# Optimization experiments

Hardware: AMD Instinct MI355X
Metric: run time of the kernel (lower is better)

## Reference

```python
import jax, jax.numpy as jnp
import numpy as np

N_MET, N_RXN, N_GENE = 2534, 4881, 6607
E, P, D = 262144, 131072, 256
LN_EPS = 1e-5


def _segment_mean(x, idx, n):
    s = jax.ops.segment_sum(x, idx, num_segments=n)
    c = jax.ops.segment_sum(jnp.ones((idx.shape[0],), x.dtype), idx, num_segments=n)
    return s / jnp.maximum(c, 1.0)[:, None]


def _hyperconv(x, eattr, node, edge, stoich, W, We, att, b):
    # PyG-style HypergraphConv with stoichiometry as incidence weight + attention.
    xp = x @ W                      # [N_MET, D]
    ep = eattr @ We                 # [N_RXN, D]
    xi = xp[node]                   # [E, D] gather
    ej = ep[edge]                   # [E, D] gather
    logits = jax.nn.leaky_relu(jnp.concatenate([xi, ej], axis=-1) @ att, 0.2)  # [E]
    m = jax.ops.segment_max(logits, edge, num_segments=N_RXN)
    ex = jnp.exp(logits - m[edge])
    ssum = jax.ops.segment_sum(ex, edge, num_segments=N_RXN)
    alpha = ex / (ssum[edge] + 1e-16)           # softmax per hyperedge
    w = stoich * alpha                           # [E]
    ones = jnp.ones_like(stoich)
    Bc = jax.ops.segment_sum(ones, edge, num_segments=N_RXN)   # nodes per edge
    me = jax.ops.segment_sum(w[:, None] * xi, edge, num_segments=N_RXN)
    me = me / jnp.maximum(Bc, 1.0)[:, None]      # node -> hyperedge
    Dc = jax.ops.segment_sum(ones, node, num_segments=N_MET)   # edges per node
    out = jax.ops.segment_sum(w[:, None] * me[edge], node, num_segments=N_MET)
    out = out / jnp.maximum(Dc, 1.0)[:, None]    # hyperedge -> node
    return out + b


def _layernorm(z, g, b):
    mu = jnp.mean(z, axis=-1, keepdims=True)
    var = jnp.mean(jnp.square(z - mu), axis=-1, keepdims=True)
    return (z - mu) / jnp.sqrt(var + LN_EPS) * g + b


def _renorm(emb):
    # nn.Embedding(max_norm=1.0): clamp row norms to <= 1
    n = jnp.linalg.norm(emb, axis=-1, keepdims=True)
    return emb * jnp.minimum(1.0, 1.0 / (n + 1e-12))


def setup_inputs() -> dict:
    key = jax.random.key(0)
    ks = jax.random.split(key, 16)
    s = 1.0 / np.sqrt(D)
    return {
        "he_node": jax.random.randint(ks[0], (E,), 0, N_MET),
        "he_edge": jax.random.randint(ks[1], (E,), 0, N_RXN),
        "stoich": jax.random.normal(ks[2], (E,), dtype=jnp.float32),
        "gene_x": jax.random.normal(ks[3], (N_GENE, D), dtype=jnp.float32),
        "rtg_rxn": jax.random.randint(ks[4], (P,), 0, N_RXN),
        "rtg_gene": jax.random.randint(ks[5], (P,), 0, N_GENE),
        "emb_table": jax.random.normal(ks[6], (N_MET, D), dtype=jnp.float32) * 0.02,
        "W0": jax.random.normal(ks[7], (D, D), dtype=jnp.float32) * s,
        "We0": jax.random.normal(ks[8], (D, D), dtype=jnp.float32) * s,
        "att0": jax.random.normal(ks[9], (2 * D,), dtype=jnp.float32) * s,
        "b0": jnp.zeros((D,), jnp.float32),
        "W1": jax.random.normal(ks[10], (D, D), dtype=jnp.float32) * s,
        "We1": jax.random.normal(ks[11], (D, D), dtype=jnp.float32) * s,
        "att1": jax.random.normal(ks[12], (2 * D,), dtype=jnp.float32) * s,
        "b1": jnp.zeros((D,), jnp.float32),
        "ln_g": jnp.ones((D,), jnp.float32),
        "ln_b": jnp.zeros((D,), jnp.float32),
    }


def reference(he_node, he_edge, stoich, gene_x, rtg_rxn, rtg_gene, emb_table,
              W0, We0, att0, b0, W1, We1, att1, b1, ln_g, ln_b):
    met = _renorm(emb_table)                                    # [N_MET, D]
    # gene -> reaction scatter-mean (flattened reaction_to_genes dict)
    rxn_emb = _segment_mean(gene_x[rtg_gene], rtg_rxn, N_RXN)   # [N_RXN, D]
    # layer 0 (no skip on first layer)
    cur = jnp.tanh(_hyperconv(met, rxn_emb, he_node, he_edge, stoich, W0, We0, att0, b0))
    # layer 1 with skip + layernorm
    nxt = jnp.tanh(_hyperconv(cur, rxn_emb, he_node, he_edge, stoich, W1, We1, att1, b1))
    cur = _layernorm(nxt + cur, ln_g, ln_b)
    # metabolite -> reaction scatter-mean over incidences
    rxn_final = _segment_mean(cur[he_node], he_edge, N_RXN)     # [N_RXN, D]
    # reaction -> gene scatter-mean
    gene_emb = _segment_mean(rxn_final[rtg_rxn], rtg_gene, N_GENE)  # [N_GENE, D]
    return gene_emb
```

## Files before the change

kernel.cpp:

```cpp
#include <hip/hip_runtime.h>
#include <math.h>

#define DD 256
static constexpr int N_MET  = 2534;
static constexpr int N_RXN  = 4881;
static constexpr int N_GENE = 6607;
static constexpr int NE     = 262144;
static constexpr int NP     = 131072;

static constexpr int NCHUNK = 256;
static constexpr int NBE    = 77;
static constexpr int NBN    = 80;
static constexpr int CHS    = 80;
static constexpr int GEMM_BLOCKS = (N_MET + 15) / 16;

__device__ __forceinline__ float waveSum(float v) {
  #pragma unroll
  for (int o = 32; o > 0; o >>= 1) v += __shfl_xor(v, o, 64);
  return v;
}
__device__ __forceinline__ float waveMax(float v) {
  #pragma unroll
  for (int o = 32; o > 0; o >>= 1) v = fmaxf(v, __shfl_xor(v, o, 64));
  return v;
}
__device__ __forceinline__ int   bcasti(int v, int l)   { return __builtin_amdgcn_readlane(v, l); }
__device__ __forceinline__ float bcastf(float v, int l) {
  return __int_as_float(__builtin_amdgcn_readlane(__float_as_int(v), l));
}

__global__ __launch_bounds__(1024) void KH_k(
    const int* __restrict__ he_node, const int* __restrict__ he_edge,
    const int* __restrict__ rtg_rxn, const int* __restrict__ rtg_gene,
    int* cntE, int* cntN, int* cntR, int* cntG,
    int* __restrict__ chE, int* __restrict__ chN,
    const float* __restrict__ We0, const float* __restrict__ att0,
    const float* __restrict__ We1, const float* __restrict__ att1,
    float* __restrict__ ve0, float* __restrict__ ve1) {
  int blk = blockIdx.x, tid = threadIdx.x;
  if (blk < 32) {
    int wid = blk * 16 + (tid >> 6);
    int lane = tid & 63;
    const float* We = (wid < 256) ? We0 : We1;
    const float* at = (wid < 256) ? att0 : att1;
    int r = wid & 255;
    float4 a = ((const float4*)(We + (size_t)r * DD))[lane];
    float4 v = ((const float4*)(at + DD))[lane];
    float s = waveSum(a.x * v.x + a.y * v.y + a.z * v.z + a.w * v.w);
    if (lane == 0) ((wid < 256) ? ve0 : ve1)[r] = s;
    return;
  }
  int c = blk - 32;
  __shared__ int hE[NBE], hN[NBN];
  if (tid < NBE) hE[tid] = 0;
  if (tid >= 128 && tid < 128 + NBN) hN[tid - 128] = 0;
  __syncthreads();
  int i = c * 1024 + tid;
  int n = he_node[i], e = he_edge[i];
  atomicAdd(&cntE[e], 1); atomicAdd(&cntN[n], 1);
  atomicAdd(&hE[e >> 6], 1); atomicAdd(&hN[n >> 5], 1);
  if (i < NP) { atomicAdd(&cntR[rtg_rxn[i]], 1); atomicAdd(&cntG[rtg_gene[i]], 1); }
  __syncthreads();
  if (tid < NBE) chE[c * CHS + tid] = hE[tid];
  if (tid >= 128 && tid < 128 + NBN) chN[c * CHS + (tid - 128)] = hN[tid - 128];
}

__global__ __launch_bounds__(1024) void KScan_k(
    const int* c0, int n0, int* o0, int* u0,
    const int* c1, int n1, int* o1, int* u1,
    const int* c2, int n2, int* o2, int* u2,
    const int* c3, int n3, int* o3, int* u3,
    int* __restrict__ chE, int* __restrict__ chN,
    const float* __restrict__ gene_x,
    const float* __restrict__ ve0, const float* __restrict__ ve1,
    float* __restrict__ gdot0, float* __restrict__ gdot1) {
  int blk = blockIdx.x, tid = threadIdx.x;
  if (blk < 4) {
    const int* cnt; int n; int* offs; int* cur;
    if      (blk == 0) { cnt = c0; n = n0; offs = o0; cur = u0; }
    else if (blk == 1) { cnt = c1; n = n1; offs = o1; cur = u1; }
    else if (blk == 2) { cnt = c2; n = n2; offs = o2; cur = u2; }
    else               { cnt = c3; n = n3; offs = o3; cur = u3; }
    __shared__ int part[1024];
    int base = tid * 8;
    int v[8]; int s = 0;
    #pragma unroll
    for (int j = 0; j < 8; ++j) { int x = (base + j < n) ? cnt[base + j] : 0; v[j] = x; s += x; }
    part[tid] = s;
    __syncthreads();
    for (int o = 1; o < 1024; o <<= 1) {
      int t = (tid >= o) ? part[tid - o] : 0;
      __syncthreads();
      part[tid] += t;
      __syncthreads();
    }
    int ex = part[tid] - s;
    #pragma unroll
    for (int j = 0; j < 8; ++j) {
      if (base + j < n) { offs[base + j] = ex; cur[base + j] = ex; ex += v[j]; }
    }
    if (tid == 1023) offs[n] = part[1023];
    return;
  }
  if (blk < 14) {
    int colw = (blk - 4) * 16 + (tid >> 6);
    int lane = tid & 63;
    if (colw >= 160) return;
    int side = colw >= 80;
    int b = colw - side * 80;
    int* ch = side ? chN : chE;
    int v[4]; int s = 0;
    int cbase = lane * 4;
    #pragma unroll
    for (int k = 0; k < 4; ++k) { v[k] = ch[(cbase + k) * CHS + b]; s += v[k]; }
    int inc = s;
    #pragma unroll
    for (int o = 1; o < 64; o <<= 1) { int t = __shfl_up(inc, o, 64); if (lane >= o) inc += t; }
    int ex = inc - s;
    #pragma unroll
    for (int k = 0; k < 4; ++k) { int t = v[k]; ch[(cbase + k) * CHS + b] = ex; ex += t; }
    return;
  }
  int wid = (blk - 14) * 16 + (tid >> 6);
  int lane = tid & 63;
  if (wid >= N_GENE) return;
  float4 a  = ((const float4*)gene_x)[(size_t)wid * 64 + lane];
  float4 v0 = ((const float4*)ve0)[lane];
  float4 v1 = ((const float4*)ve1)[lane];
  float s0 = waveSum(a.x * v0.x + a.y * v0.y + a.z * v0.z + a.w * v0.w);
  float s1 = waveSum(a.x * v1.x + a.y * v1.y + a.z * v1.z + a.w * v1.w);
  if (lane == 0) { gdot0[wid] = s0; gdot1[wid] = s1; }
}

__global__ __launch_bounds__(1024) void KP1_k(
    const int* __restrict__ he_node, const int* __restrict__ he_edge,
    const float* __restrict__ stoich,
    const int* __restrict__ offsE, const int* __restrict__ offsN,
    const int* __restrict__ chE, const int* __restrict__ chN,
    int4* __restrict__ scrE, int4* __restrict__ scrN,
    const int* __restrict__ rtg_rxn, const int* __restrict__ rtg_gene,
    int* curR, int* __restrict__ geneR,
    int* curG, int* __restrict__ rxnG) {
  int blk = blockIdx.x, tid = threadIdx.x;
  if (blk < NCHUNK) {
    __shared__ int cursE[NBE], cursN[NBN];
    int c = blk;
    if (tid < NBE) cursE[tid] = offsE[64 * tid] + chE[c * CHS + tid];
    if (tid >= 128 && tid < 128 + NBN) {
      int t = tid - 128;
      cursN[t] = offsN[32 * t] + chN[c * CHS + t];
    }
    __syncthreads();
    int i = c * 1024 + tid;
    int n = he_node[i], e = he_edge[i];
    int st = __float_as_int(stoich[i]);
    int dE = atomicAdd(&cursE[e >> 6], 1);
    scrE[dE] = make_int4(e, n, st, 0);
    int dN = atomicAdd(&cursN[n >> 5], 1);
    scrN[dN] = make_int4(n, e, st, 0);
  } else {
    int i = (blk - NCHUNK) * 1024 + tid;
    int r = rtg_rxn[i], g = rtg_gene[i];
    int pa = atomicAdd(&curR[r], 1); geneR[pa] = g;
    int pb = atomicAdd(&curG[g], 1); rxnG[pb] = r;
  }
}

template <bool RENORM>
__device__ __forceinline__ void gemm_body(const float* __restrict__ X,
                                          const float* __restrict__ W,
                                          const float* __restrict__ att,
                                          float* __restrict__ Y,
                                          float* __restrict__ sn, int M, int r0) {
  __shared__ float Xs[256][20];
  __shared__ float red[4][16];
  __shared__ float scl[16];
  int tid = threadIdx.x;
  int w = tid >> 6, lane = tid & 63;
  float xv[16];
  #pragma unroll
  for (int i = 0; i < 16; ++i) {
    int r = r0 + i;
    xv[i] = (r < M) ? X[(size_t)r * DD + tid] : 0.f;
  }
  if (RENORM) {
    #pragma unroll
    for (int i = 0; i < 16; ++i) {
      float v = waveSum(xv[i] * xv[i]);
      if (lane == 0) red[w][i] = v;
    }
    __syncthreads();
    if (tid < 16) {
      float t = red[0][tid] + red[1][tid] + red[2][tid] + red[3][tid];
      scl[tid] = fminf(1.f, 1.f / (sqrtf(t) + 1e-12f));
    }
    __syncthreads();
    #pragma unroll
    for (int i = 0; i < 16; ++i) xv[i] *= scl[i];
  }
  #pragma unroll
  for (int i = 0; i < 16; ++i) Xs[tid][i] = xv[i];
  __syncthreads();
  float acc[16];
  #pragma unroll
  for (int i = 0; i < 16; ++i) acc[i] = 0.f;
  const float* wp = W + tid;
  #pragma unroll 8
  for (int k = 0; k < 256; ++k) {
    float wv = wp[(size_t)k * DD];
    const float4* xr = reinterpret_cast<const float4*>(&Xs[k][0]);
    float4 a0 = xr[0], a1 = xr[1], a2 = xr[2], a3 = xr[3];
    acc[0]  += a0.x * wv; acc[1]  += a0.y * wv; acc[2]  += a0.z * wv; acc[3]  += a0.w * wv;
    acc[4]  += a1.x * wv; acc[5]  += a1.y * wv; acc[6]  += a1.z * wv; acc[7]  += a1.w * wv;
    acc[8]  += a2.x * wv; acc[9]  += a2.y * wv; acc[10] += a2.z * wv; acc[11] += a2.w * wv;
    acc[12] += a3.x * wv; acc[13] += a3.y * wv; acc[14] += a3.z * wv; acc[15] += a3.w * wv;
  }
  #pragma unroll
  for (int i = 0; i < 16; ++i) {
    int r = r0 + i;
    if (r < M) Y[(size_t)r * DD + tid] = acc[i];
  }
  float av = att[tid];
  __syncthreads();
  #pragma unroll
  for (int i = 0; i < 16; ++i) {
    float v = waveSum(acc[i] * av);
    if (lane == 0) red[w][i] = v;
  }
  __syncthreads();
  if (tid < 16) {
    int r = r0 + tid;
    if (r < M) sn[r] = red[0][tid] + red[1][tid] + red[2][tid] + red[3][tid];
  }
}

__global__ __launch_bounds__(256) void KP2_k(
    const int* __restrict__ offsE, const int* __restrict__ offsN,
    const int4* __restrict__ scrE, const int4* __restrict__ scrN,
    int2* __restrict__ payE, int2* __restrict__ payN,
    const float* __restrict__ emb, const float* __restrict__ W0,
    const float* __restrict__ att0, float* __restrict__ xp, float* __restrict__ sn) {
  int blk = blockIdx.x, tid = threadIdx.x;
  if (blk < NBE) {
    __shared__ int curs[64];
    int b = blk;
    int elo = 64 * b;
    int ecnt = min(64, N_RXN - elo);
    if (tid < ecnt) curs[tid] = offsE[elo + tid];
    __syncthreads();
    int lo = offsE[elo], hi = offsE[elo + ecnt];
    for (int j = lo + tid; j < hi; j += 256) {
      int4 r = scrE[j];
      int slot = atomicAdd(&curs[r.x - elo], 1);
      payE[slot] = make_int2(r.y, r.z);
    }
  } else if (blk < NBE + NBN) {
    __shared__ int curs[32];
    int b = blk - NBE;
    int nlo = 32 * b;
    int ncnt = min(32, N_MET - nlo);
    if (tid < ncnt) curs[tid] = offsN[nlo + tid];
    __syncthreads();
    int lo = offsN[nlo], hi = offsN[nlo + ncnt];
    for (int j = lo + tid; j < hi; j += 256) {
      int4 r = scrN[j];
      int slot = atomicAdd(&curs[r.x - nlo], 1);
      payN[slot] = make_int2(r.y, r.z);
    }
  } else {
    gemm_body<true>(emb, W0, att0, xp, sn, N_MET, (blk - NBE - NBN) * 16);
  }
}

__global__ __launch_bounds__(256) void gemm1_k(const float* __restrict__ X,
                                               const float* __restrict__ W,
                                               const float* __restrict__ att,
                                               float* __restrict__ Y,
                                               float* __restrict__ sn, int M) {
  gemm_body<false>(X, W, att, Y, sn, M, blockIdx.x * 16);
}

__device__ __forceinline__ void gatherAcc(float4& acc, const float4* __restrict__ src4,
                                          const int (&rv)[4], const float (&wv)[4],
                                          int nc, int lane) {
  #pragma unroll
  for (int c = 0; c < 4; ++c) {
    int lim = nc - c * 64; if (lim > 64) lim = 64;
    for (int t = 0; t < lim; t += 16) {
      float4 a[16]; float w[16];
      #pragma unroll
      for (int q = 0; q < 16; ++q) {
        int   n = bcasti(rv[c], t + q);
        w[q]    = bcastf(wv[c], t + q);
        a[q]    = src4[(size_t)n * 64 + lane];
      }
      #pragma unroll
      for (int q = 0; q < 16; ++q) {
        acc.x += w[q] * a[q].x; acc.y += w[q] * a[q].y;
        acc.z += w[q] * a[q].z; acc.w += w[q] * a[q].w;
      }
    }
  }
}

template <int STRIDE>
__global__ __launch_bounds__(256) void seg_mean_k(const int* __restrict__ offs,
                                                  const int* __restrict__ pay,
                                                  const float* __restrict__ src,
                                                  float* __restrict__ dst, int nseg) {
  int wid = (blockIdx.x * 256 + threadIdx.x) >> 6;
  int lane = threadIdx.x & 63;
  if (wid >= nseg) return;
  int beg = offs[wid], end = offs[wid + 1];
  int cnt = end - beg;
  int nc = cnt < 256 ? cnt : 256;
  int rv[4]; float wv[4];
  #pragma unroll
  for (int c = 0; c < 4; ++c) {
    int j = c * 64 + lane;
    if (j < nc) { rv[c] = pay[(size_t)(beg + j) * STRIDE]; wv[c] = 1.f; }
    else        { rv[c] = 0;                               wv[c] = 0.f; }
  }
  float4 acc = make_float4(0.f, 0.f, 0.f, 0.f);
  gatherAcc(acc, (const float4*)src, rv, wv, nc, lane);
  for (int j = 256; j < cnt; ++j) {
    int n = pay[(size_t)(beg + j) * STRIDE];
    float4 a = ((const float4*)src)[(size_t)n * 64 + lane];
    acc.x += a.x; acc.y += a.y; acc.z += a.z; acc.w += a.w;
  }
  float inv = 1.f / (float)(cnt > 1 ? cnt : 1);
  float4 o; o.x = acc.x * inv; o.y = acc.y * inv; o.z = acc.z * inv; o.w = acc.w * inv;
  ((float4*)dst)[(size_t)wid * 64 + lane] = o;
}

__global__ __launch_bounds__(256) void me_k(const int* __restrict__ offs,
                                            const int2* __restrict__ payE,
                                            const float* __restrict__ sn,
                                            const int* __restrict__ offsR,
                                            const int* __restrict__ geneR,
                                            const float* __restrict__ gdot,
                                            const float* __restrict__ xp,
                                            float* __restrict__ me,
                                            float4* __restrict__ rstat) {
  int wid = (blockIdx.x * 256 + threadIdx.x) >> 6;
  int lane = threadIdx.x & 63;
  if (wid >= N_RXN) return;
  int rb = offsR[wid], re = offsR[wid + 1];
  float sacc = 0.f;
  for (int j = rb + lane; j < re; j += 64) sacc += gdot[geneR[j]];
  int rc = re - rb;
  float ser = waveSum(sacc) / (float)(rc > 1 ? rc : 1);

  int beg = offs[wid], end = offs[wid + 1];
  int cnt = end - beg;
  int nc = cnt < 256 ? cnt : 256;
  int nv[4]; float wv[4]; float stv[4];
  float lmax = -1e30f;
  #pragma unroll
  for (int c = 0; c < 4; ++c) {
    int j = c * 64 + lane;
    if (j < nc) {
      int2 p = payE[beg + j];
      float l = sn[p.x] + ser;
      l = (l >= 0.f) ? l : 0.2f * l;
      nv[c] = p.x; wv[c] = l; stv[c] = __int_as_float(p.y);
      lmax = fmaxf(lmax, l);
    } else { nv[c] = 0; wv[c] = -1e30f; stv[c] = 0.f; }
  }
  for (int j = 256 + lane; j < cnt; j += 64) {
    int2 p = payE[beg + j];
    float l = sn[p.x] + ser;
    l = (l >= 0.f) ? l : 0.2f * l;
    lmax = fmaxf(lmax, l);
  }
  float m = waveMax(lmax);
  float s = 0.f;
  #pragma unroll
  for (int c = 0; c < 4; ++c) {
    if (c * 64 + lane < nc) { float e = expf(wv[c] - m); wv[c] = e; s += e; }
    else wv[c] = 0.f;
  }
  for (int j = 256 + lane; j < cnt; j += 64) {
    int2 p = payE[beg + j];
    float l = sn[p.x] + ser;
    l = (l >= 0.f) ? l : 0.2f * l;
    s += expf(l - m);
  }
  s = waveSum(s);
  float invS = 1.f / (s + 1e-16f);
  #pragma unroll
  for (int c = 0; c < 4; ++c) {
    if (c * 64 + lane < nc) wv[c] = stv[c] * wv[c] * invS;
  }
  if (lane == 0) rstat[wid] = make_float4(ser, m, invS, 0.f);
  float4 acc = make_float4(0.f, 0.f, 0.f, 0.f);
  gatherAcc(acc, (const float4*)xp, nv, wv, nc, lane);
  for (int j = 256; j < cnt; ++j) {
    int2 p = payE[beg + j];
    float l = sn[p.x] + ser;
    l = (l >= 0.f) ? l : 0.2f * l;
    float w = __int_as_float(p.y) * expf(l - m) * invS;
    float4 a = ((const float4*)xp)[(size_t)p.x * 64 + lane];
    acc.x += w * a.x; acc.y += w * a.y; acc.z += w * a.z; acc.w += w * a.w;
  }
  float invB = 1.f / (float)(cnt > 1 ? cnt : 1);
  float4 o; o.x = acc.x * invB; o.y = acc.y * invB; o.z = acc.z * invB; o.w = acc.w * invB;
  ((float4*)me)[(size_t)wid * 64 + lane] = o;
}

template <bool LN>
__global__ __launch_bounds__(256) void out_k(const int* __restrict__ offs,
                                             const int2* __restrict__ payN,
                                             const float* __restrict__ sn,
                                             const float4* __restrict__ rstat,
                                             const float* __restrict__ me,
                                             const float* __restrict__ bias,
                                             const float* __restrict__ ln_g,
                                             const float* __restrict__ ln_b,
                                             float* __restrict__ cur) {
  int wid = (blockIdx.x * 256 + threadIdx.x) >> 6;
  int lane = threadIdx.x & 63;
  if (wid >= N_MET) return;
  int beg = offs[wid], end = offs[wid + 1];
  int cnt = end - beg;
  int nc = cnt < 256 ? cnt : 256;
  float sn_n = sn[wid];
  int rv[4]; float wv[4];
  #pragma unroll
  for (int c = 0; c < 4; ++c) {
    int j = c * 64 + lane;
    if (j < nc) {
      int2 p = payN[beg + j];
      float4 st = rstat[p.x];
      float l = sn_n + st.x;
      l = (l >= 0.f) ? l : 0.2f * l;
      rv[c] = p.x;
      wv[c] = __int_as_float(p.y) * expf(l - st.y) * st.z;
    } else { rv[c] = 0; wv[c] = 0.f; }
  }
  float4 acc = make_float4(0.f, 0.f, 0.f, 0.f);
  gatherAcc(acc, (const float4*)me, rv, wv, nc, lane);
  for (int j = 256; j < cnt; ++j) {
    int2 p = payN[beg + j];
    float4 st = rstat[p.x];
    float l = sn_n + st.x;
    l = (l >= 0.f) ? l : 0.2f * l;
    float w = __int_as_float(p.y) * expf(l - st.y) * st.z;
    float4 a = ((const float4*)me)[(size_t)p.x * 64 + lane];
    acc.x += w * a.x; acc.y += w * a.y; acc.z += w * a.z; acc.w += w * a.w;
  }
  float invD = 1.f / (float)(cnt > 1 ? cnt : 1);
  float4 b4 = ((const float4*)bias)[lane];
  float4 o;
  o.x = tanhf(acc.x * invD + b4.x);
  o.y = tanhf(acc.y * invD + b4.y);
  o.z = tanhf(acc.z * invD + b4.z);
  o.w = tanhf(acc.w * invD + b4.w);
  float4* cur4 = (float4*)cur;
  if (!LN) {
    cur4[(size_t)wid * 64 + lane] = o;
    return;
  }
  float4 p = cur4[(size_t)wid * 64 + lane];
  float4 z; z.x = o.x + p.x; z.y = o.y + p.y; z.z = o.z + p.z; z.w = o.w + p.w;
  float mu = waveSum(z.x + z.y + z.z + z.w) * (1.f / 256.f);
  float4 zc; zc.x = z.x - mu; zc.y = z.y - mu; zc.z = z.z - mu; zc.w = z.w - mu;
  float var = waveSum(zc.x * zc.x + zc.y * zc.y + zc.z * zc.z + zc.w * zc.w) * (1.f / 256.f);
  float rs = 1.f / sqrtf(var + 1e-5f);
  float4 g4 = ((const float4*)ln_g)[lane];
  float4 be4 = ((const float4*)ln_b)[lane];
  float4 r;
  r.x = zc.x * rs * g4.x + be4.x;
  r.y = zc.y * rs * g4.y + be4.y;
  r.z = zc.z * rs * g4.z + be4.z;
  r.w = zc.w * rs * g4.w + be4.w;
  cur4[(size_t)wid * 64 + lane] = r;
}

extern "C" void kernel_launch(void* const* d_in, const int* in_sizes, int n_in,
                              void* d_out, int out_size, void* d_ws, size_t ws_size,
                              hipStream_t stream) {
  const int*   he_node = (const int*)d_in[0];
  const int*   he_edge = (const int*)d_in[1];
  const float* stoich  = (const float*)d_in[2];
  const float* gene_x  = (const float*)d_in[3];
  const int*   rtg_rxn = (const int*)d_in[4];
  const int*   rtg_gene= (const int*)d_in[5];
  const float* emb     = (const float*)d_in[6];
  const float* W0      = (const float*)d_in[7];
  const float* We0     = (const float*)d_in[8];
  const float* att0    = (const float*)d_in[9];
  const float* b0      = (const float*)d_in[10];
  const float* W1      = (const float*)d_in[11];
  const float* We1     = (const float*)d_in[12];
  const float* att1    = (const float*)d_in[13];
  const float* b1      = (const float*)d_in[14];
  const float* ln_g    = (const float*)d_in[15];
  const float* ln_b    = (const float*)d_in[16];
  float* out = (float*)d_out;

  char* base = (char*)d_ws;
  size_t off = 0;
  auto carve = [&](size_t bytes) -> char* {
    char* p = base + off;
    off += (bytes + 255) & ~(size_t)255;
    return p;
  };
  float*  xp    = (float*)carve((size_t)N_MET * DD * 4);
  float*  me    = (float*)carve((size_t)N_RXN * DD * 4);
  float*  cur   = (float*)carve((size_t)N_MET * DD * 4);
  float*  rxnf  = (float*)carve((size_t)N_RXN * DD * 4);
  float*  sn    = (float*)carve((size_t)N_MET * 4);
  float*  ve0   = (float*)carve(DD * 4);
  float*  ve1   = (float*)carve(DD * 4);
  float*  gdot0 = (float*)carve((size_t)N_GENE * 4);
  float*  gdot1 = (float*)carve((size_t)N_GENE * 4);
  float4* rstat = (float4*)carve((size_t)N_RXN * 16);
  int* cnts = (int*)carve((size_t)(N_RXN + N_MET + N_RXN + N_GENE) * 4);
  int* cntE = cnts;
  int* cntN = cntE + N_RXN;
  int* cntR = cntN + N_MET;
  int* cntG = cntR + N_RXN;
  int*  offsE = (int*)carve((N_RXN + 1) * 4);
  int*  curE  = (int*)carve(N_RXN * 4);
  int2* payE  = (int2*)carve((size_t)NE * 8);
  int*  offsN = (int*)carve((N_MET + 1) * 4);
  int*  curN  = (int*)carve(N_MET * 4);
  int2* payN  = (int2*)carve((size_t)NE * 8);
  int*  offsR = (int*)carve((N_RXN + 1) * 4);
  int*  curR  = (int*)carve(N_RXN * 4);
  int*  geneR = (int*)carve((size_t)NP * 4);
  int*  offsG = (int*)carve((N_GENE + 1) * 4);
  int*  curG  = (int*)carve(N_GENE * 4);
  int*  rxnG  = (int*)carve((size_t)NP * 4);
  int4* scrE  = (int4*)carve((size_t)NE * 16);
  int4* scrN  = (int4*)carve((size_t)NE * 16);
  int*  chE   = (int*)carve((size_t)NCHUNK * CHS * 4);
  int*  chN   = (int*)carve((size_t)NCHUNK * CHS * 4);

  hipMemsetAsync(cnts, 0, (size_t)(N_RXN + N_MET + N_RXN + N_GENE) * 4, stream);

  KH_k<<<32 + NCHUNK, 1024, 0, stream>>>(
      he_node, he_edge, rtg_rxn, rtg_gene, cntE, cntN, cntR, cntG,
      chE, chN, We0, att0, We1, att1, ve0, ve1);

  int gdot_blocks = (N_GENE + 15) / 16;
  KScan_k<<<14 + gdot_blocks, 1024, 0, stream>>>(
      cntE, N_RXN, offsE, curE,
      cntN, N_MET, offsN, curN,
      cntR, N_RXN, offsR, curR,
      cntG, N_GENE, offsG, curG,
      chE, chN, gene_x, ve0, ve1, gdot0, gdot1);

  KP1_k<<<NCHUNK + NP / 1024, 1024, 0, stream>>>(
      he_node, he_edge, stoich, offsE, offsN, chE, chN, scrE, scrN,
      rtg_rxn, rtg_gene, curR, geneR, curG, rxnG);

  KP2_k<<<NBE + NBN + GEMM_BLOCKS, 256, 0, stream>>>(
      offsE, offsN, scrE, scrN, payE, payN, emb, W0, att0, xp, sn);

  me_k<<<(N_RXN + 3) / 4, 256, 0, stream>>>(offsE, payE, sn, offsR, geneR, gdot0,
                                            xp, me, rstat);
  out_k<false><<<(N_MET + 3) / 4, 256, 0, stream>>>(offsN, payN, sn, rstat, me, b0,
                                                    nullptr, nullptr, cur);

  gemm1_k<<<GEMM_BLOCKS, 256, 0, stream>>>(cur, W1, att1, xp, sn, N_MET);
  me_k<<<(N_RXN + 3) / 4, 256, 0, stream>>>(offsE, payE, sn, offsR, geneR, gdot1,
                                            xp, me, rstat);
  out_k<true><<<(N_MET + 3) / 4, 256, 0, stream>>>(offsN, payN, sn, rstat, me, b1,
                                                   ln_g, ln_b, cur);

  seg_mean_k<2><<<(N_RXN + 3) / 4, 256, 0, stream>>>(offsE, (const int*)payE, cur, rxnf, N_RXN);
  seg_mean_k<1><<<(N_GENE + 3) / 4, 256, 0, stream>>>(offsG, rxnG, rxnf, out, N_GENE);
}
```

Baseline: 228.3 us.

## Replace gene-reaction CSR build with binned two-pass sort and atomic per-reaction sums

The per-reaction gene CSR (curR/geneR) is removed. The sum of gene dot products per reaction is now accumulated with float atomics into seAcc0/seAcc1 during the partition pass, and me_k reads that scalar instead of walking gene lists. The gene-side CSR (rxnG) now uses the same chunk-histogram plus bucket-scatter scheme as the E/N sides, replacing per-element global atomics. This trims scan work and per-wave gather loops, at the cost of extra global float atomics and non-deterministic summation order.

```diff
diff --git a/kernel.cpp b/kernel.cpp
--- a/kernel.cpp
+++ b/kernel.cpp
@@ -9,10 +9,13 @@
 static constexpr int NP     = 131072;
 
 static constexpr int NCHUNK = 256;
+static constexpr int NCHG   = 128;
 static constexpr int NBE    = 77;
 static constexpr int NBN    = 80;
+static constexpr int NBG    = 104;
 static constexpr int CHS    = 80;
 static constexpr int GEMM_BLOCKS = (N_MET + 15) / 16;
+static constexpr int KP2_GEMM0 = NBE + NBN + NBG;
 
 __device__ __forceinline__ float waveSum(float v) {
   #pragma unroll
@@ -33,7 +36,7 @@
     const int* __restrict__ he_node, const int* __restrict__ he_edge,
     const int* __restrict__ rtg_rxn, const int* __restrict__ rtg_gene,
     int* cntE, int* cntN, int* cntR, int* cntG,
-    int* __restrict__ chE, int* __restrict__ chN,
+    int* __restrict__ chE, int* __restrict__ chN, int* __restrict__ chG,
     const float* __restrict__ We0, const float* __restrict__ att0,
     const float* __restrict__ We1, const float* __restrict__ att1,
     float* __restrict__ ve0, float* __restrict__ ve1) {
@@ -51,36 +54,40 @@
     return;
   }
   int c = blk - 32;
-  __shared__ int hE[NBE], hN[NBN];
+  __shared__ int hE[NBE], hN[NBN], hG[NBG];
   if (tid < NBE) hE[tid] = 0;
   if (tid >= 128 && tid < 128 + NBN) hN[tid - 128] = 0;
+  if (tid >= 256 && tid < 256 + NBG) hG[tid - 256] = 0;
   __syncthreads();
   int i = c * 1024 + tid;
   int n = he_node[i], e = he_edge[i];
   atomicAdd(&cntE[e], 1); atomicAdd(&cntN[n], 1);
   atomicAdd(&hE[e >> 6], 1); atomicAdd(&hN[n >> 5], 1);
-  if (i < NP) { atomicAdd(&cntR[rtg_rxn[i]], 1); atomicAdd(&cntG[rtg_gene[i]], 1); }
+  if (c < NCHG) {
+    int r = rtg_rxn[i], g = rtg_gene[i];
+    atomicAdd(&cntR[r], 1); atomicAdd(&cntG[g], 1);
+    atomicAdd(&hG[g >> 6], 1);
+  }
   __syncthreads();
   if (tid < NBE) chE[c * CHS + tid] = hE[tid];
   if (tid >= 128 && tid < 128 + NBN) chN[c * CHS + (tid - 128)] = hN[tid - 128];
+  if (c < NCHG && tid >= 256 && tid < 256 + NBG) chG[c * NBG + (tid - 256)] = hG[tid - 256];
 }
 
 __global__ __launch_bounds__(1024) void KScan_k(
-    const int* c0, int n0, int* o0, int* u0,
-    const int* c1, int n1, int* o1, int* u1,
-    const int* c2, int n2, int* o2, int* u2,
-    const int* c3, int n3, int* o3, int* u3,
-    int* __restrict__ chE, int* __restrict__ chN,
+    const int* __restrict__ cntE, int* __restrict__ offsE,
+    const int* __restrict__ cntN, int* __restrict__ offsN,
+    const int* __restrict__ cntG, int* __restrict__ offsG,
+    int* __restrict__ chE, int* __restrict__ chN, int* __restrict__ chG,
     const float* __restrict__ gene_x,
     const float* __restrict__ ve0, const float* __restrict__ ve1,
     float* __restrict__ gdot0, float* __restrict__ gdot1) {
   int blk = blockIdx.x, tid = threadIdx.x;
-  if (blk < 4) {
-    const int* cnt; int n; int* offs; int* cur;
-    if      (blk == 0) { cnt = c0; n = n0; offs = o0; cur = u0; }
-    else if (blk == 1) { cnt = c1; n = n1; offs = o1; cur = u1; }
-    else if (blk == 2) { cnt = c2; n = n2; offs = o2; cur = u2; }
-    else               { cnt = c3; n = n3; offs = o3; cur = u3; }
+  if (blk < 3) {
+    const int* cnt; int n; int* offs;
+    if      (blk == 0) { cnt = cntE; n = N_RXN;  offs = offsE; }
+    else if (blk == 1) { cnt = cntN; n = N_MET;  offs = offsN; }
+    else               { cnt = cntG; n = N_GENE; offs = offsG; }
     __shared__ int part[1024];
     int base = tid * 8;
     int v[8]; int s = 0;
@@ -97,31 +104,44 @@
     int ex = part[tid] - s;
     #pragma unroll
     for (int j = 0; j < 8; ++j) {
-      if (base + j < n) { offs[base + j] = ex; cur[base + j] = ex; ex += v[j]; }
+      if (base + j < n) { offs[base + j] = ex; ex += v[j]; }
     }
     if (tid == 1023) offs[n] = part[1023];
     return;
   }
-  if (blk < 14) {
-    int colw = (blk - 4) * 16 + (tid >> 6);
+  if (blk < 20) {
+    int colw = (blk - 3) * 16 + (tid >> 6);
     int lane = tid & 63;
-    if (colw >= 160) return;
-    int side = colw >= 80;
-    int b = colw - side * 80;
-    int* ch = side ? chN : chE;
-    int v[4]; int s = 0;
-    int cbase = lane * 4;
-    #pragma unroll
-    for (int k = 0; k < 4; ++k) { v[k] = ch[(cbase + k) * CHS + b]; s += v[k]; }
-    int inc = s;
-    #pragma unroll
-    for (int o = 1; o < 64; o <<= 1) { int t = __shfl_up(inc, o, 64); if (lane >= o) inc += t; }
-    int ex = inc - s;
-    #pragma unroll
-    for (int k = 0; k < 4; ++k) { int t = v[k]; ch[(cbase + k) * CHS + b] = ex; ex += t; }
+    if (colw < NBE + NBN) {
+      int side = colw >= NBE;
+      int b = colw - side * NBE;
+      int* ch = side ? chN : chE;
+      int v[4]; int s = 0;
+      int cbase = lane * 4;
+      #pragma unroll
+      for (int k = 0; k < 4; ++k) { v[k] = ch[(cbase + k) * CHS + b]; s += v[k]; }
+      int inc = s;
+      #pragma unroll
+      for (int o = 1; o < 64; o <<= 1) { int t = __shfl_up(inc, o, 64); if (lane >= o) inc += t; }
+      int ex = inc - s;
+      #pragma unroll
+      for (int k = 0; k < 4; ++k) { int t = v[k]; ch[(cbase + k) * CHS + b] = ex; ex += t; }
+    } else if (colw < NBE + NBN + NBG) {
+      int b = colw - NBE - NBN;
+      int v[2]; int s = 0;
+      int cbase = lane * 2;
+      #pragma unroll
+      for (int k = 0; k < 2; ++k) { v[k] = chG[(cbase + k) * NBG + b]; s += v[k]; }
+      int inc = s;
+      #pragma unroll
+      for (int o = 1; o < 64; o <<= 1) { int t = __shfl_up(inc, o, 64); if (lane >= o) inc += t; }
+      int ex = inc - s;
+      #pragma unroll
+      for (int k = 0; k < 2; ++k) { int t = v[k]; chG[(cbase + k) * NBG + b] = ex; ex += t; }
+    }
     return;
   }
-  int wid = (blk - 14) * 16 + (tid >> 6);
+  int wid = (blk - 20) * 16 + (tid >> 6);
   int lane = tid & 63;
   if (wid >= N_GENE) return;
   float4 a  = ((const float4*)gene_x)[(size_t)wid * 64 + lane];
@@ -136,33 +156,38 @@
     const int* __restrict__ he_node, const int* __restrict__ he_edge,
     const float* __restrict__ stoich,
     const int* __restrict__ offsE, const int* __restrict__ offsN,
+    const int* __restrict__ offsG,
     const int* __restrict__ chE, const int* __restrict__ chN,
-    int4* __restrict__ scrE, int4* __restrict__ scrN,
+    const int* __restrict__ chG,
+    int4* __restrict__ scrE, int4* __restrict__ scrN, int2* __restrict__ scrG,
     const int* __restrict__ rtg_rxn, const int* __restrict__ rtg_gene,
-    int* curR, int* __restrict__ geneR,
-    int* curG, int* __restrict__ rxnG) {
-  int blk = blockIdx.x, tid = threadIdx.x;
-  if (blk < NCHUNK) {
-    __shared__ int cursE[NBE], cursN[NBN];
-    int c = blk;
-    if (tid < NBE) cursE[tid] = offsE[64 * tid] + chE[c * CHS + tid];
-    if (tid >= 128 && tid < 128 + NBN) {
-      int t = tid - 128;
-      cursN[t] = offsN[32 * t] + chN[c * CHS + t];
-    }
-    __syncthreads();
-    int i = c * 1024 + tid;
-    int n = he_node[i], e = he_edge[i];
-    int st = __float_as_int(stoich[i]);
-    int dE = atomicAdd(&cursE[e >> 6], 1);
-    scrE[dE] = make_int4(e, n, st, 0);
-    int dN = atomicAdd(&cursN[n >> 5], 1);
-    scrN[dN] = make_int4(n, e, st, 0);
-  } else {
-    int i = (blk - NCHUNK) * 1024 + tid;
+    const float* __restrict__ gdot0, const float* __restrict__ gdot1,
+    float* __restrict__ seAcc0, float* __restrict__ seAcc1) {
+  int c = blockIdx.x, tid = threadIdx.x;
+  __shared__ int cursE[NBE], cursN[NBN], cursG[NBG];
+  if (tid < NBE) cursE[tid] = offsE[64 * tid] + chE[c * CHS + tid];
+  if (tid >= 128 && tid < 128 + NBN) {
+    int t = tid - 128;
+    cursN[t] = offsN[32 * t] + chN[c * CHS + t];
+  }
+  if (c < NCHG && tid >= 256 && tid < 256 + NBG) {
+    int t = tid - 256;
+    cursG[t] = offsG[64 * t] + chG[c * NBG + t];
+  }
+  __syncthreads();
+  int i = c * 1024 + tid;
+  int n = he_node[i], e = he_edge[i];
+  int st = __float_as_int(stoich[i]);
+  int dE = atomicAdd(&cursE[e >> 6], 1);
+  scrE[dE] = make_int4(e, n, st, 0);
+  int dN = atomicAdd(&cursN[n >> 5], 1);
+  scrN[dN] = make_int4(n, e, st, 0);
+  if (c < NCHG) {
     int r = rtg_rxn[i], g = rtg_gene[i];
-    int pa = atomicAdd(&curR[r], 1); geneR[pa] = g;
-    int pb = atomicAdd(&curG[g], 1); rxnG[pb] = r;
+    int dG = atomicAdd(&cursG[g >> 6], 1);
+    scrG[dG] = make_int2(g, r);
+    atomicAdd(&seAcc0[r], gdot0[g]);
+    atomicAdd(&seAcc1[r], gdot1[g]);
   }
 }
 
@@ -236,15 +261,16 @@
 
 __global__ __launch_bounds__(256) void KP2_k(
     const int* __restrict__ offsE, const int* __restrict__ offsN,
+    const int* __restrict__ offsG,
     const int4* __restrict__ scrE, const int4* __restrict__ scrN,
-    int2* __restrict__ payE, int2* __restrict__ payN,
+    const int2* __restrict__ scrG,
+    int2* __restrict__ payE, int2* __restrict__ payN, int* __restrict__ rxnG,
     const float* __restrict__ emb, const float* __restrict__ W0,
     const float* __restrict__ att0, float* __restrict__ xp, float* __restrict__ sn) {
   int blk = blockIdx.x, tid = threadIdx.x;
   if (blk < NBE) {
     __shared__ int curs[64];
-    int b = blk;
-    int elo = 64 * b;
+    int elo = 64 * blk;
     int ecnt = min(64, N_RXN - elo);
     if (tid < ecnt) curs[tid] = offsE[elo + tid];
     __syncthreads();
@@ -267,8 +293,21 @@
       int slot = atomicAdd(&curs[r.x - nlo], 1);
       payN[slot] = make_int2(r.y, r.z);
     }
+  } else if (blk < KP2_GEMM0) {
+    __shared__ int curs[64];
+    int b = blk - NBE - NBN;
+    int glo = 64 * b;
+    int gcnt = min(64, N_GENE - glo);
+    if (tid < gcnt) curs[tid] = offsG[glo + tid];
+    __syncthreads();
+    int lo = offsG[glo], hi = offsG[glo + gcnt];
+    for (int j = lo + tid; j < hi; j += 256) {
+      int2 r = scrG[j];
+      int slot = atomicAdd(&curs[r.x - glo], 1);
+      rxnG[slot] = r.y;
+    }
   } else {
-    gemm_body<true>(emb, W0, att0, xp, sn, N_MET, (blk - NBE - NBN) * 16);
+    gemm_body<true>(emb, W0, att0, xp, sn, N_MET, (blk - KP2_GEMM0) * 16);
   }
 }
 
@@ -336,20 +375,16 @@
 __global__ __launch_bounds__(256) void me_k(const int* __restrict__ offs,
                                             const int2* __restrict__ payE,
                                             const float* __restrict__ sn,
-                                            const int* __restrict__ offsR,
-                                            const int* __restrict__ geneR,
-                                            const float* __restrict__ gdot,
+                                            const float* __restrict__ seAcc,
+                                            const int* __restrict__ cntR,
                                             const float* __restrict__ xp,
                                             float* __restrict__ me,
                                             float4* __restrict__ rstat) {
   int wid = (blockIdx.x * 256 + threadIdx.x) >> 6;
   int lane = threadIdx.x & 63;
   if (wid >= N_RXN) return;
-  int rb = offsR[wid], re = offsR[wid + 1];
-  float sacc = 0.f;
-  for (int j = rb + lane; j < re; j += 64) sacc += gdot[geneR[j]];
-  int rc = re - rb;
-  float ser = waveSum(sacc) / (float)(rc > 1 ? rc : 1);
+  int rc = cntR[wid];
+  float ser = seAcc[wid] / (float)(rc > 1 ? rc : 1);
 
   int beg = offs[wid], end = offs[wid + 1];
   int cnt = end - beg;
@@ -516,56 +551,53 @@
   float*  gdot0 = (float*)carve((size_t)N_GENE * 4);
   float*  gdot1 = (float*)carve((size_t)N_GENE * 4);
   float4* rstat = (float4*)carve((size_t)N_RXN * 16);
-  int* cnts = (int*)carve((size_t)(N_RXN + N_MET + N_RXN + N_GENE) * 4);
-  int* cntE = cnts;
-  int* cntN = cntE + N_RXN;
-  int* cntR = cntN + N_MET;
-  int* cntG = cntR + N_RXN;
+  int ztot = N_RXN + N_MET + N_RXN + N_GENE + 2 * N_RXN;
+  int* zbase = (int*)carve((size_t)ztot * 4);
+  int*   cntE   = zbase;
+  int*   cntN   = cntE + N_RXN;
+  int*   cntR   = cntN + N_MET;
+  int*   cntG   = cntR + N_RXN;
+  float* seAcc0 = (float*)(cntG + N_GENE);
+  float* seAcc1 = seAcc0 + N_RXN;
   int*  offsE = (int*)carve((N_RXN + 1) * 4);
-  int*  curE  = (int*)carve(N_RXN * 4);
   int2* payE  = (int2*)carve((size_t)NE * 8);
   int*  offsN = (int*)carve((N_MET + 1) * 4);
-  int*  curN  = (int*)carve(N_MET * 4);
   int2* payN  = (int2*)carve((size_t)NE * 8);
-  int*  offsR = (int*)carve((N_RXN + 1) * 4);
-  int*  curR  = (int*)carve(N_RXN * 4);
-  int*  geneR = (int*)carve((size_t)NP * 4);
   int*  offsG = (int*)carve((N_GENE + 1) * 4);
-  int*  curG  = (int*)carve(N_GENE * 4);
   int*  rxnG  = (int*)carve((size_t)NP * 4);
   int4* scrE  = (int4*)carve((size_t)NE * 16);
   int4* scrN  = (int4*)carve((size_t)NE * 16);
+  int2* scrG  = (int2*)carve((size_t)NP * 8);
   int*  chE   = (int*)carve((size_t)NCHUNK * CHS * 4);
   int*  chN   = (int*)carve((size_t)NCHUNK * CHS * 4);
-
-  hipMemsetAsync(cnts, 0, (size_t)(N_RXN + N_MET + N_RXN + N_GENE) * 4, stream);
+  int*  chG   = (int*)carve((size_t)NCHG * NBG * 4);
+
+  hipMemsetAsync(zbase, 0, (size_t)ztot * 4, stream);
 
   KH_k<<<32 + NCHUNK, 1024, 0, stream>>>(
       he_node, he_edge, rtg_rxn, rtg_gene, cntE, cntN, cntR, cntG,
-      chE, chN, We0, att0, We1, att1, ve0, ve1);
+      chE, chN, chG, We0, att0, We1, att1, ve0, ve1);
 
   int gdot_blocks = (N_GENE + 15) / 16;
-  KScan_k<<<14 + gdot_blocks, 1024, 0, stream>>>(
-      cntE, N_RXN, offsE, curE,
-      cntN, N_MET, offsN, curN,
-      cntR, N_RXN, offsR, curR,
-      cntG, N_GENE, offsG, curG,
-      chE, chN, gene_x, ve0, ve1, gdot0, gdot1);
-
-  KP1_k<<<NCHUNK + NP / 1024, 1024, 0, stream>>>(
-      he_node, he_edge, stoich, offsE, offsN, chE, chN, scrE, scrN,
-      rtg_rxn, rtg_gene, curR, geneR, curG, rxnG);
-
-  KP2_k<<<NBE + NBN + GEMM_BLOCKS, 256, 0, stream>>>(
-      offsE, offsN, scrE, scrN, payE, payN, emb, W0, att0, xp, sn);
-
-  me_k<<<(N_RXN + 3) / 4, 256, 0, stream>>>(offsE, payE, sn, offsR, geneR, gdot0,
+  KScan_k<<<20 + gdot_blocks, 1024, 0, stream>>>(
+      cntE, offsE, cntN, offsN, cntG, offsG,
+      chE, chN, chG, gene_x, ve0, ve1, gdot0, gdot1);
+
+  KP1_k<<<NCHUNK, 1024, 0, stream>>>(
+      he_node, he_edge, stoich, offsE, offsN, offsG, chE, chN, chG,
+      scrE, scrN, scrG, rtg_rxn, rtg_gene, gdot0, gdot1, seAcc0, seAcc1);
+
+  KP2_k<<<KP2_GEMM0 + GEMM_BLOCKS, 256, 0, stream>>>(
+      offsE, offsN, offsG, scrE, scrN, scrG, payE, payN, rxnG,
+      emb, W0, att0, xp, sn);
+
+  me_k<<<(N_RXN + 3) / 4, 256, 0, stream>>>(offsE, payE, sn, seAcc0, cntR,
                                             xp, me, rstat);
   out_k<false><<<(N_MET + 3) / 4, 256, 0, stream>>>(offsN, payN, sn, rstat, me, b0,
                                                     nullptr, nullptr, cur);
 
   gemm1_k<<<GEMM_BLOCKS, 256, 0, stream>>>(cur, W1, att1, xp, sn, N_MET);
-  me_k<<<(N_RXN + 3) / 4, 256, 0, stream>>>(offsE, payE, sn, offsR, geneR, gdot1,
+  me_k<<<(N_RXN + 3) / 4, 256, 0, stream>>>(offsE, payE, sn, seAcc1, cntR,
                                             xp, me, rstat);
   out_k<true><<<(N_MET + 3) / 4, 256, 0, stream>>>(offsN, payN, sn, rstat, me, b1,
                                                    ln_g, ln_b, cur);
```

Result: no change. 229.1 us (+0.4%).
